# Kernel optimization log

Measured on AMD Instinct MI355X. Metric: run time of the kernel, lower is better.

Reference implementation:

```python
import jax, jax.numpy as jnp
import numpy as np

N_FEATS = 32
EMBED_D = 128
BATCH = 16384
SELF_INTERACTION = False


def setup_inputs() -> dict:
    key = jax.random.key(0)
    x = jax.random.normal(key, (BATCH, N_FEATS, EMBED_D), dtype=jnp.float32)
    return {"x": x}


def reference(x):
    # x: [B, N, D] -- the stacked feature embeddings (tf.stack(inputs, axis=1))
    B, N, D = x.shape
    # dot_products: [B, N, N]
    dot = jnp.einsum('bnd,bmd->bnm', x, x)
    k = 0 if SELF_INTERACTION else 1
    iu, ju = jnp.triu_indices(N, k=k)  # upper-triangular (row-major order matches tf.boolean_mask)
    # gather pairwise interactions -> [B, N*(N-1)/2] (or N*(N+1)/2 with self-interaction)
    flat = dot[:, iu, ju]
    return flat
```

## Files before the change

### kernel.cpp

```cpp
#include <hip/hip_runtime.h>


#define WAVES_PER_BLOCK 4
#define F4_PER_BATCH 1024
#define OUT_PER_BATCH 496

__global__ __launch_bounds__(256, 2)
void soi_gram_kernel(const float* __restrict__ x, float* __restrict__ out) {
    const int wave = threadIdx.x >> 6;
    const int lane = threadIdx.x & 63;
    const int b = blockIdx.x * WAVES_PER_BLOCK + wave;

    __shared__ float4 lds[WAVES_PER_BLOCK * F4_PER_BATCH];
    float4* myLds = &lds[wave * F4_PER_BATCH];

    const float4* xb = reinterpret_cast<const float4*>(x) + (size_t)b * F4_PER_BATCH;
#pragma unroll
    for (int k = 0; k < 16; ++k) {
        const int f4 = (k << 6) + lane;
        const int i  = f4 >> 5;
        const int d4 = f4 & 31;
        const int qs = d4 ^ ((i >> 3) << 1);
        myLds[i * 32 + qs] = xb[f4];
    }
    asm volatile("s_waitcnt lgkmcnt(0)" ::: "memory");

    const int chunk = lane & 3;
    const int tj = (lane >> 2) & 3;
    const int ti = lane >> 4;
    const int arow0 = ti << 3;
    const int brow0 = tj << 3;
    const int aswz = ti << 1;
    const int bswz = tj << 1;

    float acc[8][8];
#pragma unroll
    for (int r = 0; r < 8; ++r)
#pragma unroll
        for (int c = 0; c < 8; ++c) acc[r][c] = 0.0f;

#pragma unroll
    for (int dq = 0; dq < 8; ++dq) {
        const int d4 = chunk + (dq << 2);
        float4 a4[8], b4[8];
#pragma unroll
        for (int r = 0; r < 8; ++r)
            a4[r] = myLds[(arow0 + r) * 32 + (d4 ^ aswz)];
#pragma unroll
        for (int r = 0; r < 8; ++r)
            b4[r] = myLds[(brow0 + r) * 32 + (d4 ^ bswz)];
#pragma unroll
        for (int r = 0; r < 8; ++r)
#pragma unroll
            for (int c = 0; c < 8; ++c) {
                acc[r][c] += a4[r].x * b4[c].x;
                acc[r][c] += a4[r].y * b4[c].y;
                acc[r][c] += a4[r].z * b4[c].z;
                acc[r][c] += a4[r].w * b4[c].w;
            }
    }

#pragma unroll
    for (int r = 0; r < 8; ++r)
#pragma unroll
        for (int c = 0; c < 8; ++c) {
            float v = acc[r][c];
            v += __shfl_xor(v, 1);
            v += __shfl_xor(v, 2);
            acc[r][c] = v;
        }

    float* outb = out + (size_t)b * OUT_PER_BATCH;
#pragma unroll
    for (int rr = 0; rr < 2; ++rr) {
        const int r = (chunk << 1) + rr;
        const int i = arow0 + r;
        const int rowOff = 31 * i - (i * (i - 1)) / 2;
#pragma unroll
        for (int c = 0; c < 8; ++c) {
            const int j = brow0 + c;
            if (j > i) outb[rowOff + (j - i - 1)] = acc[r][c];
        }
    }
}

extern "C" void kernel_launch(void* const* d_in, const int* in_sizes, int n_in,
                              void* d_out, int out_size, void* d_ws, size_t ws_size,
                              hipStream_t stream) {
    const float* x = (const float*)d_in[0];
    float* out = (float*)d_out;
    const int batch = in_sizes[0] / (32 * 128);
    const int grid = batch / WAVES_PER_BLOCK;
    soi_gram_kernel<<<grid, 256, 0, stream>>>(x, out);
}
```

Before: 441.8 us.

## Compute per-batch Gram matrix with split-bf16 MFMA instead of FP32 FMAs

Replaces the LDS-staged FP32 scalar FMA Gram computation with 16x16x32 bf16 MFMA instructions. It splits each float into hi/lo bf16 parts and uses three products to approximate FP32 accuracy. Loads come straight from global memory into registers, which drops the LDS staging and shuffle reduction. Only the three needed 16x16 tiles are computed, skipping the lower-left block. The cost is reduced precision (no lo*lo term) and the risk of uncoalesced strided global loads.

```diff
diff --git a/kernel.cpp b/kernel.cpp
--- a/kernel.cpp
+++ b/kernel.cpp
@@ -1,85 +1,79 @@
 #include <hip/hip_runtime.h>
 
 
-#define WAVES_PER_BLOCK 4
-#define F4_PER_BATCH 1024
-#define OUT_PER_BATCH 496
+typedef __attribute__((ext_vector_type(8))) short bf16x8;
+typedef __attribute__((ext_vector_type(4))) float f32x4;
 
-__global__ __launch_bounds__(256, 2)
-void soi_gram_kernel(const float* __restrict__ x, float* __restrict__ out) {
+#define MFMA(a, b, c) __builtin_amdgcn_mfma_f32_16x16x32_bf16((a), (b), (c), 0, 0, 0)
+
+__device__ __forceinline__ void split_hi_lo(float4 v0, float4 v1,
+                                            bf16x8& hi, bf16x8& lo) {
+    float vals[8] = {v0.x, v0.y, v0.z, v0.w, v1.x, v1.y, v1.z, v1.w};
+#pragma unroll
+    for (int e = 0; e < 8; ++e) {
+        const unsigned bits = __builtin_bit_cast(unsigned, vals[e]);
+        hi[e] = (short)(bits >> 16);
+        const float hf = __builtin_bit_cast(float, bits & 0xFFFF0000u);
+        const float r = vals[e] - hf;
+        lo[e] = (short)(__builtin_bit_cast(unsigned, r) >> 16);
+    }
+}
+
+__global__ __launch_bounds__(256)
+void soi_mfma_kernel(const float* __restrict__ x, float* __restrict__ out) {
     const int wave = threadIdx.x >> 6;
     const int lane = threadIdx.x & 63;
-    const int b = blockIdx.x * WAVES_PER_BLOCK + wave;
+    const long b = (long)blockIdx.x * 4 + wave;
 
-    __shared__ float4 lds[WAVES_PER_BLOCK * F4_PER_BATCH];
-    float4* myLds = &lds[wave * F4_PER_BATCH];
+    const float* xb = x + b * 4096;
+    const int r0 = lane & 15;
+    const int c  = lane >> 4;
 
-    const float4* xb = reinterpret_cast<const float4*>(x) + (size_t)b * F4_PER_BATCH;
-#pragma unroll
-    for (int k = 0; k < 16; ++k) {
-        const int f4 = (k << 6) + lane;
-        const int i  = f4 >> 5;
-        const int d4 = f4 & 31;
-        const int qs = d4 ^ ((i >> 3) << 1);
-        myLds[i * 32 + qs] = xb[f4];
-    }
-    asm volatile("s_waitcnt lgkmcnt(0)" ::: "memory");
-
-    const int chunk = lane & 3;
-    const int tj = (lane >> 2) & 3;
-    const int ti = lane >> 4;
-    const int arow0 = ti << 3;
-    const int brow0 = tj << 3;
-    const int aswz = ti << 1;
-    const int bswz = tj << 1;
-
-    float acc[8][8];
-#pragma unroll
-    for (int r = 0; r < 8; ++r)
-#pragma unroll
-        for (int c = 0; c < 8; ++c) acc[r][c] = 0.0f;
+    f32x4 acc00 = {0.f, 0.f, 0.f, 0.f};
+    f32x4 acc01 = {0.f, 0.f, 0.f, 0.f};
+    f32x4 acc11 = {0.f, 0.f, 0.f, 0.f};
 
 #pragma unroll
-    for (int dq = 0; dq < 8; ++dq) {
-        const int d4 = chunk + (dq << 2);
-        float4 a4[8], b4[8];
-#pragma unroll
-        for (int r = 0; r < 8; ++r)
-            a4[r] = myLds[(arow0 + r) * 32 + (d4 ^ aswz)];
-#pragma unroll
-        for (int r = 0; r < 8; ++r)
-            b4[r] = myLds[(brow0 + r) * 32 + (d4 ^ bswz)];
-#pragma unroll
-        for (int r = 0; r < 8; ++r)
-#pragma unroll
-            for (int c = 0; c < 8; ++c) {
-                acc[r][c] += a4[r].x * b4[c].x;
-                acc[r][c] += a4[r].y * b4[c].y;
-                acc[r][c] += a4[r].z * b4[c].z;
-                acc[r][c] += a4[r].w * b4[c].w;
-            }
+    for (int s = 0; s < 4; ++s) {
+        const float* p0 = xb + r0 * 128 + s * 32 + c * 8;
+        const float* p1 = p0 + 16 * 128;
+        const float4 a0 = *reinterpret_cast<const float4*>(p0);
+        const float4 a1 = *reinterpret_cast<const float4*>(p0 + 4);
+        const float4 b0 = *reinterpret_cast<const float4*>(p1);
+        const float4 b1 = *reinterpret_cast<const float4*>(p1 + 4);
+
+        bf16x8 f0h, f0l, f1h, f1l;
+        split_hi_lo(a0, a1, f0h, f0l);
+        split_hi_lo(b0, b1, f1h, f1l);
+
+        acc00 = MFMA(f0h, f0h, acc00);
+        acc00 = MFMA(f0h, f0l, acc00);
+        acc00 = MFMA(f0l, f0h, acc00);
+        acc01 = MFMA(f0h, f1h, acc01);
+        acc01 = MFMA(f0h, f1l, acc01);
+        acc01 = MFMA(f0l, f1h, acc01);
+        acc11 = MFMA(f1h, f1h, acc11);
+        acc11 = MFMA(f1h, f1l, acc11);
+        acc11 = MFMA(f1l, f1h, acc11);
     }
 
+    float* outb = out + (size_t)b * 496;
+    const int j = lane & 15;
 #pragma unroll
-    for (int r = 0; r < 8; ++r)
-#pragma unroll
-        for (int c = 0; c < 8; ++c) {
-            float v = acc[r][c];
-            v += __shfl_xor(v, 1);
-            v += __shfl_xor(v, 2);
-            acc[r][c] = v;
+    for (int reg = 0; reg < 4; ++reg) {
+        const int i = (c << 2) + reg;
+        if (i < j) {
+            const int base = 31 * i - (i * (i - 1)) / 2 - i - 1;
+            outb[base + j] = acc00[reg];
         }
-
-    float* outb = out + (size_t)b * OUT_PER_BATCH;
-#pragma unroll
-    for (int rr = 0; rr < 2; ++rr) {
-        const int r = (chunk << 1) + rr;
-        const int i = arow0 + r;
-        const int rowOff = 31 * i - (i * (i - 1)) / 2;
-#pragma unroll
-        for (int c = 0; c < 8; ++c) {
-            const int j = brow0 + c;
-            if (j > i) outb[rowOff + (j - i - 1)] = acc[r][c];
+        {
+            const int base = 31 * i - (i * (i - 1)) / 2 - i - 1;
+            outb[base + 16 + j] = acc01[reg];
+        }
+        if (i < j) {
+            const int I = 16 + i;
+            const int base = 31 * I - (I * (I - 1)) / 2 - I - 1;
+            outb[base + 16 + j] = acc11[reg];
         }
     }
 }
@@ -90,6 +84,6 @@
     const float* x = (const float*)d_in[0];
     float* out = (float*)d_out;
     const int batch = in_sizes[0] / (32 * 128);
-    const int grid = batch / WAVES_PER_BLOCK;
-    soi_gram_kernel<<<grid, 256, 0, stream>>>(x, out);
+    const int grid = batch / 4;
+    soi_mfma_kernel<<<grid, 256, 0, stream>>>(x, out);
 }
```

Measured after the change: 366.4 us. 1.21x faster.
